# Performance work log

Hardware: AMD Instinct MI355X
Metric: run time of the kernel (lower is better)

## Reference

```python
import jax, jax.numpy as jnp
import numpy as np

N = 100_000      # nodes
E = 1_600_000    # edges (avg degree 16)
B = 256          # destroy samples
EDGE_SIZE = 94   # edges gathered per sample (MLP edge_Size)
EMB = 64         # embedding_dim
HID = 32         # MLP hidden_size
LAYERS = 3       # gnn_layers


def setup_inputs() -> dict:
    key = jax.random.key(0)
    ks = jax.random.split(key, 24)
    s = 0.05
    inp = {
        'coord': jax.random.normal(ks[0], (N, 2), jnp.float32),
        'edge_src': jax.random.randint(ks[1], (E,), 0, N, jnp.int32),
        'edge_dst': jax.random.randint(ks[2], (E,), 0, N, jnp.int32),
        'mask': jax.random.randint(ks[3], (B, EDGE_SIZE), 0, E, jnp.int32),
        # node_layer: Linear(2, EMB)
        'Wn': jax.random.normal(ks[4], (2, EMB), jnp.float32) * s,
        'bn': jnp.zeros((EMB,), jnp.float32),
        # gnn: LAYERS residual message-passing layers, Linear(EMB, EMB) each
        'Wgnn': jax.random.normal(ks[5], (LAYERS, EMB, EMB), jnp.float32) * s,
        'bgnn': jnp.zeros((LAYERS, EMB), jnp.float32),
        # edge_layer: Linear(2*EMB, EMB) split into src/dst halves (math-identical to cat)
        'We_src': jax.random.normal(ks[6], (EMB, EMB), jnp.float32) * s,
        'We_dst': jax.random.normal(ks[7], (EMB, EMB), jnp.float32) * s,
        'be': jnp.zeros((EMB,), jnp.float32),
        # MLP.linear: Linear(64,32) -> LeakyReLU -> Linear(32,1)
        'W1': jax.random.normal(ks[8], (EMB, HID), jnp.float32) * s,
        'b1': jnp.zeros((HID,), jnp.float32),
        'W2': jax.random.normal(ks[9], (HID, 1), jnp.float32) * s,
        'b2': jnp.zeros((1,), jnp.float32),
        # MLP.decoder: Linear(94,32) -> LeakyReLU -> Linear(32,1)
        'Wd1': jax.random.normal(ks[10], (EDGE_SIZE, HID), jnp.float32) * s,
        'bd1': jnp.zeros((HID,), jnp.float32),
        'Wd2': jax.random.normal(ks[11], (HID, 1), jnp.float32) * s,
        'bd2': jnp.zeros((1,), jnp.float32),
    }
    return inp


def reference(coord, edge_src, edge_dst, mask,
              Wn, bn, Wgnn, bgnn, We_src, We_dst, be,
              W1, b1, W2, b2, Wd1, bd1, Wd2, bd2):
    n_nodes = coord.shape[0]
    lrelu = lambda x: jax.nn.leaky_relu(x, 0.01)
    # node embedding: [N, EMB]
    h = coord @ Wn + bn
    # residual GNN message passing (gather-scatter, memory bound)
    for l in range(Wgnn.shape[0]):
        agg = jax.ops.segment_sum(h[edge_src], edge_dst, num_segments=n_nodes)
        h = h + lrelu(agg @ Wgnn[l] + bgnn[l])
    # edgewise features: Linear(cat[h_src, h_dst]) == h_src@W_a + h_dst@W_b  -> [E, EMB]
    ef = h[edge_src] @ We_src + h[edge_dst] @ We_dst + be
    # per-destroy-sample gather of 94 edge features: [B, 94, EMB]
    x = ef[mask]
    # MLP.linear over feature dim -> [B, 94]
    x = (lrelu(x @ W1 + b1) @ W2 + b2)[..., 0]
    # MLP.decoder over the 94 edges -> [B]
    out = (lrelu(x @ Wd1 + bd1) @ Wd2 + bd2)[:, 0]
    return out
```

## Files before the change

### kernel.cpp

```cpp
#include <hip/hip_runtime.h>

#define NN   100000
#define EE   1600000
#define BB   256
#define ES   94
#define EMB  64
#define HID  32
#define NB   391
#define EPB  16
#define DBINS 128

__device__ __forceinline__ float lrelu(float x) { return x > 0.f ? x : 0.01f * x; }


__global__ __launch_bounds__(256) void k_bhist(const int* __restrict__ dst,
                                               int* __restrict__ bcnt) {
    __shared__ int h[NB];
    int t = threadIdx.x;
    for (int i = t; i < NB; i += 256) h[i] = 0;
    __syncthreads();
    int e0 = blockIdx.x * 4096 + t * 16;
    if (e0 + 16 <= EE) {
        #pragma unroll
        for (int j = 0; j < 4; ++j) {
            int4 d = *(const int4*)&dst[e0 + j * 4];
            atomicAdd(&h[d.x >> 8], 1);
            atomicAdd(&h[d.y >> 8], 1);
            atomicAdd(&h[d.z >> 8], 1);
            atomicAdd(&h[d.w >> 8], 1);
        }
    } else {
        for (int e = e0; e < EE; ++e) atomicAdd(&h[dst[e] >> 8], 1);
    }
    __syncthreads();
    for (int i = t; i < NB; i += 256) if (h[i]) atomicAdd(&bcnt[i], h[i]);
}

__global__ void k_bscan(const int* __restrict__ bcnt, int* __restrict__ boff,
                        int* __restrict__ bcur, int* __restrict__ off) {
    __shared__ int sd[512];
    int t = threadIdx.x;
    int v = (t < NB) ? bcnt[t] : 0;
    sd[t] = v;
    __syncthreads();
    for (int o = 1; o < 512; o <<= 1) {
        int x = (t >= o) ? sd[t - o] : 0;
        __syncthreads();
        sd[t] += x;
        __syncthreads();
    }
    if (t < NB) { boff[t] = sd[t] - v; bcur[t] = sd[t] - v; }
    if (t == 0) { boff[NB] = EE; off[NN] = EE; }
}

__global__ __launch_bounds__(256) void k_bin(const int* __restrict__ src,
                                             const int* __restrict__ dst,
                                             int* __restrict__ bcur,
                                             int* __restrict__ bp) {
    __shared__ int h[NB];
    __shared__ int base[NB];
    int t = threadIdx.x;
    for (int i = t; i < NB; i += 256) h[i] = 0;
    __syncthreads();
    int e0 = blockIdx.x * 2048 + t * 8;
    int ve[8], vb[8], vr[8];
    if (e0 + 8 <= EE) {
        int4 s0 = *(const int4*)&src[e0];
        int4 s1 = *(const int4*)&src[e0 + 4];
        int4 d0 = *(const int4*)&dst[e0];
        int4 d1 = *(const int4*)&dst[e0 + 4];
        int ss[8] = {s0.x, s0.y, s0.z, s0.w, s1.x, s1.y, s1.z, s1.w};
        int dd[8] = {d0.x, d0.y, d0.z, d0.w, d1.x, d1.y, d1.z, d1.w};
        #pragma unroll
        for (int i = 0; i < 8; ++i) {
            int bk = dd[i] >> 8;
            vb[i] = bk;
            ve[i] = (ss[i] << 8) | (dd[i] & 255);
            vr[i] = atomicAdd(&h[bk], 1);
        }
    } else {
        #pragma unroll
        for (int i = 0; i < 8; ++i) {
            int e = e0 + i;
            if (e < EE) {
                int d = dst[e], s = src[e];
                int bk = d >> 8;
                vb[i] = bk;
                ve[i] = (s << 8) | (d & 255);
                vr[i] = atomicAdd(&h[bk], 1);
            } else vb[i] = -1;
        }
    }
    __syncthreads();
    for (int i = t; i < NB; i += 256) base[i] = h[i] ? atomicAdd(&bcur[i], h[i]) : 0;
    __syncthreads();
    #pragma unroll
    for (int i = 0; i < 8; ++i)
        if (vb[i] >= 0) bp[base[vb[i]] + vr[i]] = ve[i];
}

__global__ __launch_bounds__(256) void k_bcsr(const int* __restrict__ boff,
                                              const int* __restrict__ bp,
                                              int* __restrict__ off,
                                              int* __restrict__ csr,
                                              int* __restrict__ dcnt) {
    __shared__ int hist[256];
    __shared__ int loc[256];
    __shared__ int dh[DBINS];
    int t = threadIdx.x;
    int b = blockIdx.x;
    int e0 = boff[b], e1 = boff[b + 1];
    hist[t] = 0;
    if (t < DBINS) dh[t] = 0;
    __syncthreads();
    for (int e = e0 + t; e < e1; e += 256) atomicAdd(&hist[bp[e] & 255], 1);
    __syncthreads();
    int v = hist[t];
    loc[t] = v;
    __syncthreads();
    for (int o = 1; o < 256; o <<= 1) {
        int x = (t >= o) ? loc[t - o] : 0;
        __syncthreads();
        loc[t] += x;
        __syncthreads();
    }
    int excl = loc[t] - v;
    int n = (b << 8) + t;
    bool valid = n < NN;
    if (valid) off[n] = e0 + excl;
    hist[t] = excl;
    int d = v > DBINS - 1 ? DBINS - 1 : v;
    if (valid) atomicAdd(&dh[d], 1);
    __syncthreads();
    for (int e = e0 + t; e < e1; e += 256) {
        int pv = bp[e];
        int p = e0 + atomicAdd(&hist[pv & 255], 1);
        csr[p] = pv >> 8;
    }
    if (t < DBINS && dh[t]) atomicAdd(&dcnt[t], dh[t]);
}

__global__ void k_dscan(const int* __restrict__ dcnt, int* __restrict__ dcur) {
    __shared__ int sd[DBINS];
    int t = threadIdx.x;
    int v = dcnt[t];
    sd[t] = v;
    __syncthreads();
    for (int o = 1; o < DBINS; o <<= 1) {
        int x = (t >= o) ? sd[t - o] : 0;
        __syncthreads();
        sd[t] += x;
        __syncthreads();
    }
    dcur[t] = sd[t] - v;
}

__global__ __launch_bounds__(256) void k_dperm(const int* __restrict__ off,
                                               int* __restrict__ dcur,
                                               int* __restrict__ perm) {
    __shared__ int h[DBINS];
    __shared__ int base[DBINS];
    int t = threadIdx.x;
    if (t < DBINS) h[t] = 0;
    __syncthreads();
    int n = blockIdx.x * 256 + t;
    int d = 0, r = 0;
    if (n < NN) {
        d = off[n + 1] - off[n];
        if (d > DBINS - 1) d = DBINS - 1;
        r = atomicAdd(&h[d], 1);
    }
    __syncthreads();
    if (t < DBINS) base[t] = h[t] ? atomicAdd(&dcur[t], h[t]) : 0;
    __syncthreads();
    if (n < NN) perm[base[d] + r] = n;
}

__global__ __launch_bounds__(256) void k_gg0(const float2* __restrict__ coordv,
                                             const int* __restrict__ off,
                                             const int* __restrict__ csr,
                                             const float* __restrict__ Wn,
                                             const float* __restrict__ bn,
                                             const float* __restrict__ Wg,
                                             const float* __restrict__ bg,
                                             float* __restrict__ hout) {
    __shared__ float WgL[EMB * EMB];
    __shared__ float aggL[16][EMB + 4];
    int t = threadIdx.x;
    for (int i = t * 4; i < EMB * EMB; i += 256 * 4)
        *(float4*)&WgL[i] = *(const float4*)&Wg[i];
    int g = t >> 4;
    int r = t & 15;
    int r4 = r * 4;
    int n = blockIdx.x * 16 + g;
    int s0 = off[n], s1 = off[n + 1];
    float sx = 0.f, sy = 0.f;
    for (int e = s0 + r; e < s1; e += 16) {
        float2 c = coordv[csr[e]];
        sx += c.x; sy += c.y;
    }
    #pragma unroll
    for (int o = 8; o >= 1; o >>= 1) {
        sx += __shfl_xor(sx, o);
        sy += __shfl_xor(sy, o);
    }
    float deg = (float)(s1 - s0);
    float4 wn0 = *(const float4*)&Wn[r4];
    float4 wn1 = *(const float4*)&Wn[EMB + r4];
    float4 bnv = *(const float4*)&bn[r4];
    aggL[g][r4 + 0] = sx * wn0.x + sy * wn1.x + deg * bnv.x;
    aggL[g][r4 + 1] = sx * wn0.y + sy * wn1.y + deg * bnv.y;
    aggL[g][r4 + 2] = sx * wn0.z + sy * wn1.z + deg * bnv.z;
    aggL[g][r4 + 3] = sx * wn0.w + sy * wn1.w + deg * bnv.w;
    __syncthreads();
    float4 acc = *(const float4*)&bg[r4];
    #pragma unroll
    for (int k = 0; k < EMB; ++k) {
        float a = aggL[g][k];
        float4 w = *(const float4*)&WgL[k * EMB + r4];
        acc.x += a * w.x; acc.y += a * w.y; acc.z += a * w.z; acc.w += a * w.w;
    }
    float2 c = coordv[n];
    float4 hb;
    hb.x = c.x * wn0.x + c.y * wn1.x + bnv.x + lrelu(acc.x);
    hb.y = c.x * wn0.y + c.y * wn1.y + bnv.y + lrelu(acc.y);
    hb.z = c.x * wn0.z + c.y * wn1.z + bnv.z + lrelu(acc.z);
    hb.w = c.x * wn0.w + c.y * wn1.w + bnv.w + lrelu(acc.w);
    *(float4*)&hout[n * EMB + r4] = hb;
}

__global__ __launch_bounds__(256) void k_gg(const float* __restrict__ hin,
                                            const int* __restrict__ off,
                                            const int* __restrict__ csr,
                                            const int* __restrict__ perm,
                                            const float* __restrict__ Wg,
                                            const float* __restrict__ bg,
                                            float* __restrict__ hout) {
    __shared__ float WgL[EMB * EMB];
    __shared__ float aggL[16][EMB + 4];
    int t = threadIdx.x;
    for (int i = t * 4; i < EMB * EMB; i += 256 * 4)
        *(float4*)&WgL[i] = *(const float4*)&Wg[i];
    int g = t >> 4;
    int r4 = (t & 15) * 4;
    int n = perm[blockIdx.x * 16 + g];
    int s0 = off[n], s1 = off[n + 1];
    float ax = 0.f, ay = 0.f, az = 0.f, aw = 0.f;
    int e = s0;
    for (; e + 8 <= s1; e += 8) {
        int idx[8];
        #pragma unroll
        for (int j = 0; j < 8; ++j) idx[j] = csr[e + j];
        float4 x[8];
        #pragma unroll
        for (int j = 0; j < 8; ++j) x[j] = *(const float4*)&hin[idx[j] * EMB + r4];
        #pragma unroll
        for (int j = 0; j < 8; ++j) {
            ax += x[j].x; ay += x[j].y; az += x[j].z; aw += x[j].w;
        }
    }
    for (; e < s1; ++e) {
        int i0 = csr[e];
        float4 x0 = *(const float4*)&hin[i0 * EMB + r4];
        ax += x0.x; ay += x0.y; az += x0.z; aw += x0.w;
    }
    aggL[g][r4 + 0] = ax;
    aggL[g][r4 + 1] = ay;
    aggL[g][r4 + 2] = az;
    aggL[g][r4 + 3] = aw;
    __syncthreads();
    float4 acc = *(const float4*)&bg[r4];
    #pragma unroll
    for (int k = 0; k < EMB; ++k) {
        float a = aggL[g][k];
        float4 w = *(const float4*)&WgL[k * EMB + r4];
        acc.x += a * w.x; acc.y += a * w.y; acc.z += a * w.z; acc.w += a * w.w;
    }
    float4 hb = *(const float4*)&hin[n * EMB + r4];
    hb.x += lrelu(acc.x);
    hb.y += lrelu(acc.y);
    hb.z += lrelu(acc.z);
    hb.w += lrelu(acc.w);
    *(float4*)&hout[n * EMB + r4] = hb;
}

__global__ __launch_bounds__(256) void k_ef(
    const float* __restrict__ h, const int* __restrict__ esrc, const int* __restrict__ edst,
    const int* __restrict__ mask,
    const float* __restrict__ WeS, const float* __restrict__ WeD, const float* __restrict__ be,
    const float* __restrict__ W1, const float* __restrict__ b1,
    const float* __restrict__ W2, const float* __restrict__ b2,
    float* __restrict__ xout)
{
    __shared__ float WeSL[EMB * EMB];
    __shared__ float WeDL[EMB * EMB];
    __shared__ float W1L[EMB * HID];
    __shared__ float hsL[EPB][EMB + 4];
    __shared__ float hdL[EPB][EMB + 4];
    int t = threadIdx.x;
    for (int i = t; i < EMB * EMB / 4; i += 256) {
        ((float4*)WeSL)[i] = ((const float4*)WeS)[i];
        ((float4*)WeDL)[i] = ((const float4*)WeD)[i];
    }
    for (int i = t; i < EMB * HID / 4; i += 256) ((float4*)W1L)[i] = ((const float4*)W1)[i];
    int g = t >> 4, r = t & 15, r4 = r * 4;
    int idx = blockIdx.x * EPB + g;
    int e = mask[idx];
    int s = esrc[e], d = edst[e];
    float4 hs4 = *(const float4*)&h[s * EMB + r4];
    float4 hd4 = *(const float4*)&h[d * EMB + r4];
    *(float4*)&hsL[g][r4] = hs4;
    *(float4*)&hdL[g][r4] = hd4;
    __syncthreads();
    float4 acc = *(const float4*)&be[r4];
    #pragma unroll
    for (int k = 0; k < EMB; ++k) {
        float a = hsL[g][k];
        float c = hdL[g][k];
        float4 w1 = *(const float4*)&WeSL[k * EMB + r4];
        float4 w2 = *(const float4*)&WeDL[k * EMB + r4];
        acc.x += a * w1.x + c * w2.x;
        acc.y += a * w1.y + c * w2.y;
        acc.z += a * w1.z + c * w2.z;
        acc.w += a * w1.w + c * w2.w;
    }
    __syncthreads();
    *(float4*)&hsL[g][r4] = acc;
    __syncthreads();
    float a1 = b1[r], a2 = b1[r + 16];
    #pragma unroll
    for (int k = 0; k < EMB; ++k) {
        float ek = hsL[g][k];
        a1 += ek * W1L[k * HID + r];
        a2 += ek * W1L[k * HID + r + 16];
    }
    float y1 = lrelu(a1), y2 = lrelu(a2);
    float p = y1 * W2[r] + y2 * W2[r + 16];
    p += __shfl_xor(p, 1);
    p += __shfl_xor(p, 2);
    p += __shfl_xor(p, 4);
    p += __shfl_xor(p, 8);
    if (r == 0) xout[idx] = p + b2[0];
}

__global__ __launch_bounds__(64) void k_dec(const float* __restrict__ xout,
                                            const float* __restrict__ Wd1,
                                            const float* __restrict__ bd1,
                                            const float* __restrict__ Wd2,
                                            const float* __restrict__ bd2,
                                            float* __restrict__ out) {
    int b = blockIdx.x, t = threadIdx.x;
    float z = 0.f;
    if (t < HID) {
        float acc = bd1[t];
        for (int i = 0; i < ES; ++i) acc += xout[b * ES + i] * Wd1[i * HID + t];
        z = lrelu(acc) * Wd2[t];
    }
    z += __shfl_xor(z, 1);
    z += __shfl_xor(z, 2);
    z += __shfl_xor(z, 4);
    z += __shfl_xor(z, 8);
    z += __shfl_xor(z, 16);
    if (t == 0) out[b] = z + bd2[0];
}

extern "C" void kernel_launch(void* const* d_in, const int* in_sizes, int n_in,
                              void* d_out, int out_size, void* d_ws, size_t ws_size,
                              hipStream_t stream) {
    const float* coord = (const float*)d_in[0];
    const int*   esrc  = (const int*)d_in[1];
    const int*   edst  = (const int*)d_in[2];
    const int*   mask  = (const int*)d_in[3];
    const float* Wn    = (const float*)d_in[4];
    const float* bn    = (const float*)d_in[5];
    const float* Wgnn  = (const float*)d_in[6];
    const float* bgnn  = (const float*)d_in[7];
    const float* WeS   = (const float*)d_in[8];
    const float* WeD   = (const float*)d_in[9];
    const float* be    = (const float*)d_in[10];
    const float* W1    = (const float*)d_in[11];
    const float* b1    = (const float*)d_in[12];
    const float* W2    = (const float*)d_in[13];
    const float* b2    = (const float*)d_in[14];
    const float* Wd1   = (const float*)d_in[15];
    const float* bd1   = (const float*)d_in[16];
    const float* Wd2   = (const float*)d_in[17];
    const float* bd2   = (const float*)d_in[18];
    float* out = (float*)d_out;

    char* ws = (char*)d_ws;
    size_t o = 0;
    auto alloc = [&](size_t bytes) {
        void* p = ws + o;
        o = (o + bytes + 255) & ~(size_t)255;
        return p;
    };
    float* hA   = (float*)alloc((size_t)NN * EMB * 4);
    float* hB   = (float*)alloc((size_t)NN * EMB * 4);
    int* off    = (int*)alloc((size_t)(NN + 1) * 4);
    int* csr    = (int*)alloc((size_t)EE * 4);
    int* bp     = (int*)alloc((size_t)EE * 4);
    int* bcnt   = (int*)alloc((size_t)NB * 4);
    int* boff   = (int*)alloc((size_t)(NB + 1) * 4);
    int* bcur   = (int*)alloc((size_t)NB * 4);
    int* perm   = (int*)alloc((size_t)NN * 4);
    int* dcnt   = (int*)alloc((size_t)DBINS * 4);
    int* dcur   = (int*)alloc((size_t)DBINS * 4);
    float* xout = (float*)alloc((size_t)BB * ES * 4);
    (void)ws_size; (void)in_sizes; (void)n_in; (void)out_size;

    const float2* coordv = (const float2*)coord;

    hipMemsetAsync(bcnt, 0, NB * sizeof(int), stream);
    hipMemsetAsync(dcnt, 0, DBINS * sizeof(int), stream);
    k_bhist<<<(EE + 4095) / 4096, 256, 0, stream>>>(edst, bcnt);
    k_bscan<<<1, 512, 0, stream>>>(bcnt, boff, bcur, off);
    k_bin<<<(EE + 2047) / 2048, 256, 0, stream>>>(esrc, edst, bcur, bp);
    k_bcsr<<<NB, 256, 0, stream>>>(boff, bp, off, csr, dcnt);

    k_dscan<<<1, DBINS, 0, stream>>>(dcnt, dcur);
    k_dperm<<<(NN + 255) / 256, 256, 0, stream>>>(off, dcur, perm);

    k_gg0<<<NN / 16, 256, 0, stream>>>(coordv, off, csr, Wn, bn,
                                       Wgnn, bgnn, hA);

    k_gg<<<NN / 16, 256, 0, stream>>>(hA, off, csr, perm,
                                      Wgnn + (size_t)1 * EMB * EMB,
                                      bgnn + (size_t)1 * EMB, hB);
    k_gg<<<NN / 16, 256, 0, stream>>>(hB, off, csr, perm,
                                      Wgnn + (size_t)2 * EMB * EMB,
                                      bgnn + (size_t)2 * EMB, hA);

    k_ef<<<BB * ES / EPB, 256, 0, stream>>>(hA, esrc, edst, mask, WeS, WeD, be,
                                            W1, b1, W2, b2, xout);
    k_dec<<<BB, 64, 0, stream>>>(xout, Wd1, bd1, Wd2, bd2, out);
}
```

Baseline: 267.7 us.

## Compute last GNN layer only for nodes referenced by masked edges

Marks the source and destination nodes of the edges named in the sample mask, compacts them into a list (in degree-sorted order, reversed so high-degree nodes come first), and runs the final message-passing layer only for those nodes. This is valid because only those nodes' final embeddings feed the edge-feature stage. It adds marking, compaction and memset kernels plus a device-side count read, and replaces a full-graph layer with work on at most roughly 48K nodes. Blocks beyond the count exit early, but the grid is still sized for all nodes.

```diff
diff --git a/kernel.cpp b/kernel.cpp
--- a/kernel.cpp
+++ b/kernel.cpp
@@ -152,7 +152,7 @@
         sd[t] += x;
         __syncthreads();
     }
-    dcur[t] = sd[t] - v;
+    dcur[t] = NN - sd[t];
 }
 
 __global__ __launch_bounds__(256) void k_dperm(const int* __restrict__ off,
@@ -174,6 +174,41 @@
     if (t < DBINS) base[t] = h[t] ? atomicAdd(&dcur[t], h[t]) : 0;
     __syncthreads();
     if (n < NN) perm[base[d] + r] = n;
+}
+
+__global__ __launch_bounds__(256) void k_mark(const int* __restrict__ mask,
+                                              const int* __restrict__ esrc,
+                                              const int* __restrict__ edst,
+                                              int* __restrict__ flag) {
+    int i = blockIdx.x * 256 + threadIdx.x;
+    if (i < BB * ES) {
+        int e = mask[i];
+        flag[esrc[e]] = 1;
+        flag[edst[e]] = 1;
+    }
+}
+
+__global__ __launch_bounds__(256) void k_compact(const int* __restrict__ perm,
+                                                 const int* __restrict__ flag,
+                                                 int* __restrict__ list,
+                                                 int* __restrict__ gcnt) {
+    __shared__ int loc[256];
+    __shared__ int sbase;
+    int t = threadIdx.x;
+    int i = blockIdx.x * 256 + t;
+    int n = (i < NN) ? perm[i] : 0;
+    int f = (i < NN) ? flag[n] : 0;
+    loc[t] = f;
+    __syncthreads();
+    for (int o = 1; o < 256; o <<= 1) {
+        int x = (t >= o) ? loc[t - o] : 0;
+        __syncthreads();
+        loc[t] += x;
+        __syncthreads();
+    }
+    if (t == 255 && loc[255]) sbase = atomicAdd(gcnt, loc[255]);
+    __syncthreads();
+    if (f) list[sbase + loc[t] - 1] = n;
 }
 
 __global__ __launch_bounds__(256) void k_gg0(const float2* __restrict__ coordv,
@@ -282,6 +317,69 @@
     hb.z += lrelu(acc.z);
     hb.w += lrelu(acc.w);
     *(float4*)&hout[n * EMB + r4] = hb;
+}
+
+__global__ __launch_bounds__(256) void k_gg3(const float* __restrict__ hin,
+                                             const int* __restrict__ off,
+                                             const int* __restrict__ csr,
+                                             const int* __restrict__ list,
+                                             const int* __restrict__ gcnt,
+                                             const float* __restrict__ Wg,
+                                             const float* __restrict__ bg,
+                                             float* __restrict__ hout) {
+    __shared__ float WgL[EMB * EMB];
+    __shared__ float aggL[16][EMB + 4];
+    int cnt = *gcnt;
+    if (blockIdx.x * 16 >= cnt) return;
+    int t = threadIdx.x;
+    for (int i = t * 4; i < EMB * EMB; i += 256 * 4)
+        *(float4*)&WgL[i] = *(const float4*)&Wg[i];
+    int g = t >> 4;
+    int r4 = (t & 15) * 4;
+    int li = blockIdx.x * 16 + g;
+    bool act = li < cnt;
+    int n = act ? list[li] : 0;
+    int s0 = 0, s1 = 0;
+    if (act) { s0 = off[n]; s1 = off[n + 1]; }
+    float ax = 0.f, ay = 0.f, az = 0.f, aw = 0.f;
+    int e = s0;
+    for (; e + 8 <= s1; e += 8) {
+        int idx[8];
+        #pragma unroll
+        for (int j = 0; j < 8; ++j) idx[j] = csr[e + j];
+        float4 x[8];
+        #pragma unroll
+        for (int j = 0; j < 8; ++j) x[j] = *(const float4*)&hin[idx[j] * EMB + r4];
+        #pragma unroll
+        for (int j = 0; j < 8; ++j) {
+            ax += x[j].x; ay += x[j].y; az += x[j].z; aw += x[j].w;
+        }
+    }
+    for (; e < s1; ++e) {
+        int i0 = csr[e];
+        float4 x0 = *(const float4*)&hin[i0 * EMB + r4];
+        ax += x0.x; ay += x0.y; az += x0.z; aw += x0.w;
+    }
+    aggL[g][r4 + 0] = ax;
+    aggL[g][r4 + 1] = ay;
+    aggL[g][r4 + 2] = az;
+    aggL[g][r4 + 3] = aw;
+    __syncthreads();
+    float4 acc = *(const float4*)&bg[r4];
+    #pragma unroll
+    for (int k = 0; k < EMB; ++k) {
+        float a = aggL[g][k];
+        float4 w = *(const float4*)&WgL[k * EMB + r4];
+        acc.x += a * w.x; acc.y += a * w.y; acc.z += a * w.z; acc.w += a * w.w;
+    }
+    if (act) {
+        float4 hb = *(const float4*)&hin[n * EMB + r4];
+        hb.x += lrelu(acc.x);
+        hb.y += lrelu(acc.y);
+        hb.z += lrelu(acc.z);
+        hb.w += lrelu(acc.w);
+        *(float4*)&hout[n * EMB + r4] = hb;
+    }
 }
 
 __global__ __launch_bounds__(256) void k_ef(
@@ -406,6 +504,9 @@
     int* perm   = (int*)alloc((size_t)NN * 4);
     int* dcnt   = (int*)alloc((size_t)DBINS * 4);
     int* dcur   = (int*)alloc((size_t)DBINS * 4);
+    int* flag   = (int*)alloc((size_t)NN * 4);
+    int* list   = (int*)alloc((size_t)NN * 4);
+    int* gcnt   = (int*)alloc(256);
     float* xout = (float*)alloc((size_t)BB * ES * 4);
     (void)ws_size; (void)in_sizes; (void)n_in; (void)out_size;
 
@@ -413,6 +514,11 @@
 
     hipMemsetAsync(bcnt, 0, NB * sizeof(int), stream);
     hipMemsetAsync(dcnt, 0, DBINS * sizeof(int), stream);
+    hipMemsetAsync(flag, 0, (size_t)NN * sizeof(int), stream);
+    hipMemsetAsync(gcnt, 0, sizeof(int), stream);
+
+    k_mark<<<(BB * ES + 255) / 256, 256, 0, stream>>>(mask, esrc, edst, flag);
+
     k_bhist<<<(EE + 4095) / 4096, 256, 0, stream>>>(edst, bcnt);
     k_bscan<<<1, 512, 0, stream>>>(bcnt, boff, bcur, off);
     k_bin<<<(EE + 2047) / 2048, 256, 0, stream>>>(esrc, edst, bcur, bp);
@@ -421,15 +527,18 @@
     k_dscan<<<1, DBINS, 0, stream>>>(dcnt, dcur);
     k_dperm<<<(NN + 255) / 256, 256, 0, stream>>>(off, dcur, perm);
 
+    k_compact<<<(NN + 255) / 256, 256, 0, stream>>>(perm, flag, list, gcnt);
+
     k_gg0<<<NN / 16, 256, 0, stream>>>(coordv, off, csr, Wn, bn,
                                        Wgnn, bgnn, hA);
 
     k_gg<<<NN / 16, 256, 0, stream>>>(hA, off, csr, perm,
                                       Wgnn + (size_t)1 * EMB * EMB,
                                       bgnn + (size_t)1 * EMB, hB);
-    k_gg<<<NN / 16, 256, 0, stream>>>(hB, off, csr, perm,
-                                      Wgnn + (size_t)2 * EMB * EMB,
-                                      bgnn + (size_t)2 * EMB, hA);
+
+    k_gg3<<<(NN + 15) / 16, 256, 0, stream>>>(hB, off, csr, list, gcnt,
+                                              Wgnn + (size_t)2 * EMB * EMB,
+                                              bgnn + (size_t)2 * EMB, hA);
 
     k_ef<<<BB * ES / EPB, 256, 0, stream>>>(hA, esrc, edst, mask, WeS, WeD, be,
                                             W1, b1, W2, b2, xout);
```

Measured after the change: 249.2 us. 6.9% less time.
